# Kernel optimization log

Measured on AMD Instinct MI355X. Metric: run time of the kernel, lower is better.

## Reference

```python
import jax, jax.numpy as jnp
import numpy as np

N_NODES = 100000
N_EDGES = 3200000
IN_DIM, HID, N_LAB = 128, 64, 121


def setup_inputs() -> dict:
    key = jax.random.key(0)
    ks = jax.random.split(key, 8)
    x = jax.random.normal(ks[0], (N_NODES, IN_DIM), dtype=jnp.float32)
    edge_index = jax.random.randint(ks[1], (2, N_EDGES), 0, N_NODES, dtype=jnp.int64)
    W1 = jax.random.normal(ks[2], (IN_DIM, HID), dtype=jnp.float32) * (1.0 / np.sqrt(IN_DIM))
    b1 = jnp.zeros((HID,), dtype=jnp.float32)
    W2 = jax.random.normal(ks[3], (HID, HID), dtype=jnp.float32) * (1.0 / np.sqrt(HID))
    b2 = jnp.zeros((HID,), dtype=jnp.float32)
    Wout = jax.random.normal(ks[4], (HID, N_LAB), dtype=jnp.float32) * (1.0 / np.sqrt(HID))
    bout = jnp.zeros((N_LAB,), dtype=jnp.float32)
    return {"x": x, "edge_index": edge_index, "W1": W1, "b1": b1,
            "W2": W2, "b2": b2, "Wout": Wout, "bout": bout}


def _gcn_conv(x, W, b, src, dst, norm, n):
    # x' = D^{-1/2}(A+I)D^{-1/2} X W + b  (edges already include self-loops)
    xw = x @ W                                   # [N, out]
    msg = xw[src] * norm[:, None]                # [E+N, out] gather + scale
    agg = jax.ops.segment_sum(msg, dst, num_segments=n)  # scatter-add
    return agg + b


def reference(x, edge_index, W1, b1, W2, b2, Wout, bout):
    n = x.shape[0]
    loop = jnp.arange(n, dtype=edge_index.dtype)
    src = jnp.concatenate([edge_index[0], loop])
    dst = jnp.concatenate([edge_index[1], loop])
    # symmetric normalization (self-loops guarantee deg >= 1)
    deg = jax.ops.segment_sum(jnp.ones_like(dst, dtype=x.dtype), dst, num_segments=n)
    dinv = jax.lax.rsqrt(deg)
    norm = dinv[src] * dinv[dst]                 # [E+N]

    h = jax.nn.relu(_gcn_conv(x, W1, b1, src, dst, norm, n))
    # dropout p=0.5 is identity in eval mode (training=False)
    h = jax.nn.relu(_gcn_conv(h, W2, b2, src, dst, norm, n))
    logits = h @ Wout + bout                     # [N, num_labels]
    return logits
```

## Files before the change

### kernel.cpp

```cpp
#include <hip/hip_runtime.h>
#include <hip/hip_bf16.h>
#include <hip/hip_fp16.h>


#define IN_DIM 128
#define HID 64
#define N_LAB 121
#define NB_BLK 256

__global__ void scan1(const int* __restrict__ in, int* __restrict__ out,
                      int* __restrict__ bsums, int n) {
    __shared__ int s[256];
    int i = blockIdx.x * 256 + threadIdx.x;
    int v = (i < n) ? in[i] : 0;
    s[threadIdx.x] = v;
    __syncthreads();
    for (int off = 1; off < 256; off <<= 1) {
        int t = (threadIdx.x >= off) ? s[threadIdx.x - off] : 0;
        __syncthreads();
        s[threadIdx.x] += t;
        __syncthreads();
    }
    if (i < n) out[i] = s[threadIdx.x] - v;
    if (threadIdx.x == 255) bsums[blockIdx.x] = s[255];
}

__global__ void scan2(int* __restrict__ bsums, int nb) {
    __shared__ int s[512];
    int v = (threadIdx.x < nb) ? bsums[threadIdx.x] : 0;
    s[threadIdx.x] = v;
    __syncthreads();
    for (int off = 1; off < 512; off <<= 1) {
        int t = (threadIdx.x >= off) ? s[threadIdx.x - off] : 0;
        __syncthreads();
        s[threadIdx.x] += t;
        __syncthreads();
    }
    if (threadIdx.x < nb) bsums[threadIdx.x] = s[threadIdx.x] - v;
}

__global__ void scan_add(int* __restrict__ out, const int* __restrict__ bsums, int n) {
    int i = blockIdx.x * 256 + threadIdx.x;
    if (i < n) out[i] += bsums[blockIdx.x];
}

__global__ __launch_bounds__(256) void bucket_count(const int* __restrict__ dst,
                                                    int* __restrict__ counts,
                                                    int nbuk, int chunk, int E) {
    extern __shared__ int c[];
    for (int j = threadIdx.x; j < nbuk; j += 256) c[j] = 0;
    __syncthreads();
    int beg = blockIdx.x * chunk;
    int end = min(beg + chunk, E);
    for (int i = beg + threadIdx.x; i < end; i += 256)
        atomicAdd(&c[dst[i] >> 8], 1);
    __syncthreads();
    for (int j = threadIdx.x; j < nbuk; j += 256)
        counts[j * NB_BLK + blockIdx.x] = c[j];
}

__global__ __launch_bounds__(256) void bucket_scatter(const int* __restrict__ src,
                                                      const int* __restrict__ dst,
                                                      const int* __restrict__ base,
                                                      int* __restrict__ bucketed,
                                                      int nbuk, int chunk, int E) {
    extern __shared__ int c[];
    for (int j = threadIdx.x; j < nbuk; j += 256) c[j] = 0;
    __syncthreads();
    int beg = blockIdx.x * chunk;
    int end = min(beg + chunk, E);
    for (int i = beg + threadIdx.x; i < end; i += 256) {
        int d = dst[i];
        int b = d >> 8;
        int r = atomicAdd(&c[b], 1);
        int pos = base[b * NB_BLK + blockIdx.x] + r;
        bucketed[pos] = ((d & 255) << 17) | src[i];
    }
}

__global__ __launch_bounds__(256) void bucket_sort(const int* __restrict__ bucketed,
                                                   const int* __restrict__ base,
                                                   int* __restrict__ srcs,
                                                   int* __restrict__ row_ptr,
                                                   float* __restrict__ dinv,
                                                   int nbuk, int N, int E) {
    __shared__ int h[256];
    __shared__ int cur[256];
    int b = blockIdx.x;
    int nodeBase = b << 8;
    int s = base[b * NB_BLK];
    int e = (b == nbuk - 1) ? E : base[(b + 1) * NB_BLK];
    h[threadIdx.x] = 0;
    __syncthreads();
    for (int i = s + threadIdx.x; i < e; i += 256)
        atomicAdd(&h[bucketed[i] >> 17], 1);
    __syncthreads();
    int v = h[threadIdx.x];
    for (int off = 1; off < 256; off <<= 1) {
        int t = (threadIdx.x >= off) ? h[threadIdx.x - off] : 0;
        __syncthreads();
        h[threadIdx.x] += t;
        __syncthreads();
    }
    int excl = h[threadIdx.x] - v;
    cur[threadIdx.x] = excl;
    int node = nodeBase + threadIdx.x;
    if (node < N) {
        row_ptr[node] = s + excl;
        dinv[node] = rsqrtf((float)v + 1.0f);
    }
    if (b == nbuk - 1 && threadIdx.x == 0) row_ptr[N] = E;
    __syncthreads();
    for (int i = s + threadIdx.x; i < e; i += 256) {
        int p = bucketed[i];
        int d = p >> 17;
        int r = atomicAdd(&cur[d], 1);
        srcs[s + r] = p & 0x1FFFF;
    }
}

template <int K, int N, typename OT>
__global__ __launch_bounds__(256) void gemm_kernel(
        const float* __restrict__ A, const float* __restrict__ B,
        const float* __restrict__ bias, const float* __restrict__ rowscale,
        OT* __restrict__ C, int M) {
    constexpr int ROWS = 64;
    constexpr int NPAD = (N <= 64) ? 64 : 128;
    constexpr int CG = NPAD / 4;
    constexpr int RG = 256 / CG;
    constexpr int RPT = ROWS / RG;
    __shared__ float Bs[K * NPAD];
    __shared__ float As[ROWS * K];

    for (int i = threadIdx.x; i < K * NPAD; i += 256) {
        int c = i & (NPAD - 1);
        int k = i / NPAD;
        Bs[i] = (c < N) ? B[k * N + c] : 0.f;
    }
    const int row_base = blockIdx.x * ROWS;
    const float* Ablk = A + (size_t)row_base * K;
    int avail = (M - row_base) * K;
    if (avail > ROWS * K) avail = ROWS * K;
    const int nvec = avail >> 2;
    const float4* __restrict__ Av = (const float4*)Ablk;
    float4* Asv = (float4*)As;
    for (int i = threadIdx.x; i < nvec; i += 256) Asv[i] = Av[i];
    __syncthreads();

    const int cg = threadIdx.x % CG;
    const int rg = threadIdx.x / CG;

    float acc[RPT][4];
    #pragma unroll
    for (int j = 0; j < RPT; ++j) {
        acc[j][0] = 0.f; acc[j][1] = 0.f; acc[j][2] = 0.f; acc[j][3] = 0.f;
    }

    for (int k = 0; k < K; k += 4) {
        float4 Bq[4];
        #pragma unroll
        for (int kk = 0; kk < 4; ++kk)
            Bq[kk] = *(const float4*)&Bs[(k + kk) * NPAD + cg * 4];
        #pragma unroll
        for (int j = 0; j < RPT; ++j) {
            const float4 Aq = *(const float4*)&As[(rg + RG * j) * K + k];
            #pragma unroll
            for (int c = 0; c < 4; ++c) {
                const float b0 = ((const float*)&Bq[0])[c];
                const float b1 = ((const float*)&Bq[1])[c];
                const float b2 = ((const float*)&Bq[2])[c];
                const float b3 = ((const float*)&Bq[3])[c];
                float a = acc[j][c];
                a = fmaf(Aq.x, b0, a);
                a = fmaf(Aq.y, b1, a);
                a = fmaf(Aq.z, b2, a);
                a = fmaf(Aq.w, b3, a);
                acc[j][c] = a;
            }
        }
    }

    float bv[4];
    #pragma unroll
    for (int c = 0; c < 4; ++c) {
        int col = cg * 4 + c;
        bv[c] = (bias && col < N) ? bias[col] : 0.f;
    }

    #pragma unroll
    for (int j = 0; j < RPT; ++j) {
        const int r = row_base + rg + RG * j;
        if (r >= M) continue;
        const float sc = rowscale ? rowscale[r] : 1.0f;
        float o[4];
        #pragma unroll
        for (int c = 0; c < 4; ++c) o[c] = fmaf(acc[j][c], sc, bv[c]);
        OT* Crow = C + (size_t)r * N;
        if constexpr (sizeof(OT) == 4 && (N % 4 == 0)) {
            *(float4*)&Crow[cg * 4] = make_float4(o[0], o[1], o[2], o[3]);
        } else if constexpr (sizeof(OT) == 2 && (N % 4 == 0)) {
            __half2* p = (__half2*)&Crow[cg * 4];
            p[0] = __floats2half2_rn(o[0], o[1]);
            p[1] = __floats2half2_rn(o[2], o[3]);
        } else {
            #pragma unroll
            for (int c = 0; c < 4; ++c) {
                int col = cg * 4 + c;
                if (col < N) Crow[col] = (OT)o[c];
            }
        }
    }
}

__global__ __launch_bounds__(256) void aggregate(
        const __half* __restrict__ feat2, const int* __restrict__ rp,
        const int* __restrict__ srcs, const float* __restrict__ dinv,
        const float* __restrict__ bias, float* __restrict__ out, int N) {
    size_t gid = (size_t)blockIdx.x * blockDim.x + threadIdx.x;
    int r = (int)(gid >> 6);
    int f = (int)(gid & 63);
    if (r >= N) return;
    int beg = rp[r], end = rp[r + 1];
    float acc = __half2float(feat2[((size_t)r << 6) + f]);
    int e = beg;
    for (; e + 8 <= end; e += 8) {
        int s0 = srcs[e], s1 = srcs[e + 1], s2 = srcs[e + 2], s3 = srcs[e + 3];
        int s4 = srcs[e + 4], s5 = srcs[e + 5], s6 = srcs[e + 6], s7 = srcs[e + 7];
        float v0 = __half2float(feat2[((size_t)s0 << 6) + f]);
        float v1 = __half2float(feat2[((size_t)s1 << 6) + f]);
        float v2 = __half2float(feat2[((size_t)s2 << 6) + f]);
        float v3 = __half2float(feat2[((size_t)s3 << 6) + f]);
        float v4 = __half2float(feat2[((size_t)s4 << 6) + f]);
        float v5 = __half2float(feat2[((size_t)s5 << 6) + f]);
        float v6 = __half2float(feat2[((size_t)s6 << 6) + f]);
        float v7 = __half2float(feat2[((size_t)s7 << 6) + f]);
        acc += v0; acc += v1; acc += v2; acc += v3;
        acc += v4; acc += v5; acc += v6; acc += v7;
    }
    for (; e < end; ++e) acc += __half2float(feat2[((size_t)srcs[e] << 6) + f]);
    out[gid] = fmaxf(fmaf(acc, dinv[r], bias[f]), 0.f);
}

extern "C" void kernel_launch(void* const* d_in, const int* in_sizes, int n_in,
                              void* d_out, int out_size, void* d_ws, size_t ws_size,
                              hipStream_t stream) {
    const float* x    = (const float*)d_in[0];
    const int*   ei   = (const int*)d_in[1];
    const float* W1   = (const float*)d_in[2];
    const float* b1   = (const float*)d_in[3];
    const float* W2   = (const float*)d_in[4];
    const float* b2   = (const float*)d_in[5];
    const float* Wout = (const float*)d_in[6];
    const float* bout = (const float*)d_in[7];
    float* out = (float*)d_out;

    const int N = in_sizes[0] / IN_DIM;
    const int E = in_sizes[1] / 2;
    const int* srcI = ei;
    const int* dstI = ei + E;

    const int nbuk = (N + 255) >> 8;
    const int M1 = nbuk * NB_BLK;
    const int chunk = (E + NB_BLK - 1) / NB_BLK;

    int*    row_ptr = (int*)d_ws;
    float*  dinv    = (float*)(row_ptr + (N + 1));
    int*    counts  = (int*)(dinv + N);
    int*    base    = counts + M1;
    int*    bsums2  = base + M1;
    int*    srcs    = bsums2 + 512;
    __half* feat2   = (__half*)(srcs + E);
    float*  hbuf    = (float*)(feat2 + (size_t)N * HID);
    int*    bucketed = (int*)feat2;

    const int nbM = (M1 + 255) / 256;
    const int gemmBlocks = (N + 63) / 64;
    const int aggBlocks = (int)(((size_t)N * HID + 255) / 256);
    const size_t ldsBuk = (size_t)nbuk * sizeof(int);

    bucket_count<<<NB_BLK, 256, ldsBuk, stream>>>(dstI, counts, nbuk, chunk, E);
    scan1<<<nbM, 256, 0, stream>>>(counts, base, bsums2, M1);
    scan2<<<1, 512, 0, stream>>>(bsums2, nbM);
    scan_add<<<nbM, 256, 0, stream>>>(base, bsums2, M1);
    bucket_scatter<<<NB_BLK, 256, ldsBuk, stream>>>(srcI, dstI, base, bucketed, nbuk, chunk, E);
    bucket_sort<<<nbuk, 256, 0, stream>>>(bucketed, base, srcs, row_ptr, dinv, nbuk, N, E);

    gemm_kernel<IN_DIM, HID, __half><<<gemmBlocks, 256, 0, stream>>>(x, W1, nullptr, dinv, feat2, N);
    aggregate<<<aggBlocks, 256, 0, stream>>>(feat2, row_ptr, srcs, dinv, b1, hbuf, N);

    gemm_kernel<HID, HID, __half><<<gemmBlocks, 256, 0, stream>>>(hbuf, W2, nullptr, dinv, feat2, N);
    aggregate<<<aggBlocks, 256, 0, stream>>>(feat2, row_ptr, srcs, dinv, b2, hbuf, N);

    gemm_kernel<HID, N_LAB, float><<<gemmBlocks, 256, 0, stream>>>(hbuf, Wout, bout, nullptr, out, N);
}
```

Measured before the change: 552.1 us.

## Fuse neighbor aggregation with following dense GEMM in one kernel

Replaces the separate aggregate kernels and the following GEMMs with a fused agg_mm kernel. Each block aggregates 64 rows into LDS, then multiplies by W2 or Wout directly, so the fp32 hidden buffer is never written to or read back from global memory. The gather loop is also unrolled to 16 edges. In exchange, each block loads the full weight matrix into LDS, and per-block aggregation parallelism moves from a flat grid to 64 rows per block, which could lower occupancy because of the larger LDS footprint.

```diff
diff --git a/kernel.cpp b/kernel.cpp
--- a/kernel.cpp
+++ b/kernel.cpp
@@ -166,15 +166,11 @@
             const float4 Aq = *(const float4*)&As[(rg + RG * j) * K + k];
             #pragma unroll
             for (int c = 0; c < 4; ++c) {
-                const float b0 = ((const float*)&Bq[0])[c];
-                const float b1 = ((const float*)&Bq[1])[c];
-                const float b2 = ((const float*)&Bq[2])[c];
-                const float b3 = ((const float*)&Bq[3])[c];
                 float a = acc[j][c];
-                a = fmaf(Aq.x, b0, a);
-                a = fmaf(Aq.y, b1, a);
-                a = fmaf(Aq.z, b2, a);
-                a = fmaf(Aq.w, b3, a);
+                a = fmaf(Aq.x, ((const float*)&Bq[0])[c], a);
+                a = fmaf(Aq.y, ((const float*)&Bq[1])[c], a);
+                a = fmaf(Aq.z, ((const float*)&Bq[2])[c], a);
+                a = fmaf(Aq.w, ((const float*)&Bq[3])[c], a);
                 acc[j][c] = a;
             }
         }
@@ -212,33 +208,129 @@
     }
 }
 
-__global__ __launch_bounds__(256) void aggregate(
-        const __half* __restrict__ feat2, const int* __restrict__ rp,
+template <int NOUT, bool ROWSCALE, typename OT>
+__global__ __launch_bounds__(256) void agg_mm(
+        const __half* __restrict__ feat_in, const int* __restrict__ rp,
         const int* __restrict__ srcs, const float* __restrict__ dinv,
-        const float* __restrict__ bias, float* __restrict__ out, int N) {
-    size_t gid = (size_t)blockIdx.x * blockDim.x + threadIdx.x;
-    int r = (int)(gid >> 6);
-    int f = (int)(gid & 63);
-    if (r >= N) return;
-    int beg = rp[r], end = rp[r + 1];
-    float acc = __half2float(feat2[((size_t)r << 6) + f]);
-    int e = beg;
-    for (; e + 8 <= end; e += 8) {
-        int s0 = srcs[e], s1 = srcs[e + 1], s2 = srcs[e + 2], s3 = srcs[e + 3];
-        int s4 = srcs[e + 4], s5 = srcs[e + 5], s6 = srcs[e + 6], s7 = srcs[e + 7];
-        float v0 = __half2float(feat2[((size_t)s0 << 6) + f]);
-        float v1 = __half2float(feat2[((size_t)s1 << 6) + f]);
-        float v2 = __half2float(feat2[((size_t)s2 << 6) + f]);
-        float v3 = __half2float(feat2[((size_t)s3 << 6) + f]);
-        float v4 = __half2float(feat2[((size_t)s4 << 6) + f]);
-        float v5 = __half2float(feat2[((size_t)s5 << 6) + f]);
-        float v6 = __half2float(feat2[((size_t)s6 << 6) + f]);
-        float v7 = __half2float(feat2[((size_t)s7 << 6) + f]);
-        acc += v0; acc += v1; acc += v2; acc += v3;
-        acc += v4; acc += v5; acc += v6; acc += v7;
-    }
-    for (; e < end; ++e) acc += __half2float(feat2[((size_t)srcs[e] << 6) + f]);
-    out[gid] = fmaxf(fmaf(acc, dinv[r], bias[f]), 0.f);
+        const float* __restrict__ bias_agg, const float* __restrict__ W,
+        const float* __restrict__ bias_out, OT* __restrict__ out, int N) {
+    constexpr int NPAD = (NOUT <= 64) ? 64 : 128;
+    constexpr int CG = NPAD / 4;
+    constexpr int RG = 256 / CG;
+    constexpr int RPT = 64 / RG;
+    constexpr int HSTR = 68;
+    __shared__ float hs[64 * HSTR];
+    __shared__ float Ws[64 * NPAD];
+    __shared__ float dv[64];
+
+    for (int i = threadIdx.x; i < 64 * NPAD; i += 256) {
+        int c = i & (NPAD - 1);
+        int k = i / NPAD;
+        Ws[i] = (c < NOUT) ? W[k * NOUT + c] : 0.f;
+    }
+
+    const int row_base = blockIdx.x * 64;
+    const int f = threadIdx.x & 63;
+    const int ry = threadIdx.x >> 6;
+    const float bagg = bias_agg[f];
+
+    for (int t = 0; t < 16; ++t) {
+        const int j = ry + 4 * t;
+        const int r = row_base + j;
+        float val = 0.f;
+        if (r < N) {
+            const float di = dinv[r];
+            if (f == 0) dv[j] = di;
+            int beg = rp[r], end = rp[r + 1];
+            float acc = __half2float(feat_in[((size_t)r << 6) + f]);
+            int e = beg;
+            for (; e + 16 <= end; e += 16) {
+                int si[16];
+                #pragma unroll
+                for (int i = 0; i < 16; ++i) si[i] = srcs[e + i];
+                float v[16];
+                #pragma unroll
+                for (int i = 0; i < 16; ++i)
+                    v[i] = __half2float(feat_in[((size_t)si[i] << 6) + f]);
+                #pragma unroll
+                for (int i = 0; i < 16; ++i) acc += v[i];
+            }
+            for (; e + 4 <= end; e += 4) {
+                int s0 = srcs[e], s1 = srcs[e + 1], s2 = srcs[e + 2], s3 = srcs[e + 3];
+                float v0 = __half2float(feat_in[((size_t)s0 << 6) + f]);
+                float v1 = __half2float(feat_in[((size_t)s1 << 6) + f]);
+                float v2 = __half2float(feat_in[((size_t)s2 << 6) + f]);
+                float v3 = __half2float(feat_in[((size_t)s3 << 6) + f]);
+                acc += v0; acc += v1; acc += v2; acc += v3;
+            }
+            for (; e < end; ++e) acc += __half2float(feat_in[((size_t)srcs[e] << 6) + f]);
+            val = fmaxf(fmaf(acc, di, bagg), 0.f);
+        } else if (f == 0) {
+            dv[j] = 0.f;
+        }
+        hs[j * HSTR + f] = val;
+    }
+    __syncthreads();
+
+    const int cg = threadIdx.x % CG;
+    const int rg = threadIdx.x / CG;
+
+    float acc[RPT][4];
+    #pragma unroll
+    for (int j = 0; j < RPT; ++j) {
+        acc[j][0] = 0.f; acc[j][1] = 0.f; acc[j][2] = 0.f; acc[j][3] = 0.f;
+    }
+    for (int k = 0; k < 64; k += 4) {
+        float4 Bq[4];
+        #pragma unroll
+        for (int kk = 0; kk < 4; ++kk)
+            Bq[kk] = *(const float4*)&Ws[(k + kk) * NPAD + cg * 4];
+        #pragma unroll
+        for (int j = 0; j < RPT; ++j) {
+            const float4 Aq = *(const float4*)&hs[(rg + RG * j) * HSTR + k];
+            #pragma unroll
+            for (int c = 0; c < 4; ++c) {
+                float a = acc[j][c];
+                a = fmaf(Aq.x, ((const float*)&Bq[0])[c], a);
+                a = fmaf(Aq.y, ((const float*)&Bq[1])[c], a);
+                a = fmaf(Aq.z, ((const float*)&Bq[2])[c], a);
+                a = fmaf(Aq.w, ((const float*)&Bq[3])[c], a);
+                acc[j][c] = a;
+            }
+        }
+    }
+
+    float bv[4];
+    #pragma unroll
+    for (int c = 0; c < 4; ++c) {
+        int col = cg * 4 + c;
+        bv[c] = (bias_out && col < NOUT) ? bias_out[col] : 0.f;
+    }
+
+    #pragma unroll
+    for (int j = 0; j < RPT; ++j) {
+        const int lr = rg + RG * j;
+        const int r = row_base + lr;
+        if (r >= N) continue;
+        const float sc = ROWSCALE ? dv[lr] : 1.0f;
+        float o[4];
+        #pragma unroll
+        for (int c = 0; c < 4; ++c) o[c] = fmaf(acc[j][c], sc, bv[c]);
+        OT* Crow = out + (size_t)r * NOUT;
+        if constexpr (sizeof(OT) == 2 && (NOUT % 4 == 0)) {
+            __half2* p = (__half2*)&Crow[cg * 4];
+            p[0] = __floats2half2_rn(o[0], o[1]);
+            p[1] = __floats2half2_rn(o[2], o[3]);
+        } else if constexpr (sizeof(OT) == 4 && (NOUT % 4 == 0)) {
+            *(float4*)&Crow[cg * 4] = make_float4(o[0], o[1], o[2], o[3]);
+        } else {
+            #pragma unroll
+            for (int c = 0; c < 4; ++c) {
+                int col = cg * 4 + c;
+                if (col < NOUT) Crow[col] = (OT)o[c];
+            }
+        }
+    }
 }
 
 extern "C" void kernel_launch(void* const* d_in, const int* in_sizes, int n_in,
@@ -269,13 +361,12 @@
     int*    base    = counts + M1;
     int*    bsums2  = base + M1;
     int*    srcs    = bsums2 + 512;
-    __half* feat2   = (__half*)(srcs + E);
-    float*  hbuf    = (float*)(feat2 + (size_t)N * HID);
-    int*    bucketed = (int*)feat2;
+    __half* feat2a  = (__half*)(srcs + E);
+    __half* feat2b  = feat2a + (size_t)N * HID;
+    int*    bucketed = (int*)feat2a;
 
     const int nbM = (M1 + 255) / 256;
     const int gemmBlocks = (N + 63) / 64;
-    const int aggBlocks = (int)(((size_t)N * HID + 255) / 256);
     const size_t ldsBuk = (size_t)nbuk * sizeof(int);
 
     bucket_count<<<NB_BLK, 256, ldsBuk, stream>>>(dstI, counts, nbuk, chunk, E);
@@ -285,11 +376,11 @@
     bucket_scatter<<<NB_BLK, 256, ldsBuk, stream>>>(srcI, dstI, base, bucketed, nbuk, chunk, E);
     bucket_sort<<<nbuk, 256, 0, stream>>>(bucketed, base, srcs, row_ptr, dinv, nbuk, N, E);
 
-    gemm_kernel<IN_DIM, HID, __half><<<gemmBlocks, 256, 0, stream>>>(x, W1, nullptr, dinv, feat2, N);
-    aggregate<<<aggBlocks, 256, 0, stream>>>(feat2, row_ptr, srcs, dinv, b1, hbuf, N);
-
-    gemm_kernel<HID, HID, __half><<<gemmBlocks, 256, 0, stream>>>(hbuf, W2, nullptr, dinv, feat2, N);
-    aggregate<<<aggBlocks, 256, 0, stream>>>(feat2, row_ptr, srcs, dinv, b2, hbuf, N);
-
-    gemm_kernel<HID, N_LAB, float><<<gemmBlocks, 256, 0, stream>>>(hbuf, Wout, bout, nullptr, out, N);
-}
+    gemm_kernel<IN_DIM, HID, __half><<<gemmBlocks, 256, 0, stream>>>(x, W1, nullptr, dinv, feat2a, N);
+
+    agg_mm<HID, true, __half><<<gemmBlocks, 256, 0, stream>>>(
+        feat2a, row_ptr, srcs, dinv, b1, W2, nullptr, feat2b, N);
+
+    agg_mm<N_LAB, false, float><<<gemmBlocks, 256, 0, stream>>>(
+        feat2b, row_ptr, srcs, dinv, b2, Wout, bout, out, N);
+}
```

Result: slower. 655.6 us (+18.7%).
